# Optimization experiments

Hardware: AMD Instinct MI355X
Metric: run time of the kernel (lower is better)

The kernel has to match this reference:

```python
import jax, jax.numpy as jnp
import numpy as np

H = 128          # hidden_size
D = 128          # input_size
N_LEAVES = 262144  # 2**18 leaves -> complete binary tree, 18 reduction levels


def setup_inputs() -> dict:
    key = jax.random.key(0)
    k1, k2, k3, k4, k5 = jax.random.split(key, 5)
    s = 0.05
    return {
        "leaf_features": jax.random.normal(k1, (N_LEAVES, D), jnp.float32),
        "W_x": jax.random.normal(k2, (D, 5 * H), jnp.float32) * s,  # torch Linear weight (transposed)
        "b_x": jax.random.normal(k3, (5 * H,), jnp.float32) * s,
        "U_L": jax.random.normal(k4, (H, 5 * H), jnp.float32) * s,  # no bias, per module
        "U_R": jax.random.normal(k5, (H, 5 * H), jnp.float32) * s,
    }


def _cell(gates, left_c=None, right_c=None):
    # gates: [n, 5H] -> chunk(5, dim=1) order: i, f_L, f_R, o, u
    i, f_L, f_R, o, u = jnp.split(gates, 5, axis=1)
    c = jax.nn.sigmoid(i) * jnp.tanh(u)
    if left_c is not None:
        c = c + jax.nn.sigmoid(f_L) * left_c
    if right_c is not None:
        c = c + jax.nn.sigmoid(f_R) * right_c
    h = jax.nn.sigmoid(o) * jnp.tanh(c)
    return h, c


def reference(leaf_features, W_x, b_x, U_L, U_R):
    # Leaves: cell(feat, None, None, None, None) -> only W_x gates, all nodes batched.
    h, c = _cell(leaf_features @ W_x + b_x)  # [N_LEAVES, H]
    # Internal nodes, processed level-by-level (depth batching of the recursion).
    # Internal x = zeros -> W_x contributes only its bias b_x.
    while h.shape[0] > 1:
        gates = b_x + h[0::2] @ U_L + h[1::2] @ U_R  # [n/2, 5H]
        h, c = _cell(gates, c[0::2], c[1::2])
    return h  # root hidden state, shape (1, H)
```

## Files before the change

kernel.cpp:

```cpp
#include <hip/hip_runtime.h>
#include <hip/hip_bf16.h>
#include <stdint.h>


#define H5 640
#define HH 128
#define NLEAF 262144

typedef __attribute__((ext_vector_type(4))) float f32x4;
typedef __attribute__((ext_vector_type(8))) short bf16x8;
typedef __attribute__((ext_vector_type(4))) unsigned int u32x4;

static __device__ __forceinline__ unsigned short f2bf(float f) {
  union { float f; unsigned int i; } v; v.f = f;
  unsigned int r = v.i + 0x7FFF + ((v.i >> 16) & 1);
  return (unsigned short)(r >> 16);
}

static __device__ __forceinline__ float sigf(float x) {
  return 1.0f / (1.0f + __expf(-x));
}
static __device__ __forceinline__ float tanh_fast(float x) {
  float t = __expf(2.0f * x);
  return (t - 1.0f) / (t + 1.0f);
}

__global__ void pack_weights(const float* __restrict__ srcA,
                             const float* __restrict__ srcB,
                             int split, int KT, unsigned short* __restrict__ dst) {
  int t = blockIdx.x * blockDim.x + threadIdx.x;
  int total = 40 * KT * 64;
  if (t >= total) return;
  int lane = t & 63;
  int kf = (t >> 6) % KT;
  int nf = (t >> 6) / KT;
  int col = nf * 16 + (lane & 15);
  int k0 = kf * 32 + (lane >> 4) * 8;
  unsigned int w[4];
#pragma unroll
  for (int p = 0; p < 4; ++p) {
    int ka = k0 + 2 * p, kb = k0 + 2 * p + 1;
    float fa = (ka < split) ? srcA[(size_t)ka * H5 + col] : srcB[(size_t)(ka - split) * H5 + col];
    float fb = (kb < split) ? srcA[(size_t)kb * H5 + col] : srcB[(size_t)(kb - split) * H5 + col];
    w[p] = (unsigned int)f2bf(fa) | ((unsigned int)f2bf(fb) << 16);
  }
  u32x4* out = (u32x4*)(dst + (size_t)t * 8);
  u32x4 v; unsigned int* vp = (unsigned int*)&v;
  vp[0] = w[0]; vp[1] = w[1]; vp[2] = w[2]; vp[3] = w[3];
  *out = v;
}

__global__ void cast_leaf(const float* __restrict__ src,
                          unsigned short* __restrict__ dst, long n8) {
  long t = (long)blockIdx.x * blockDim.x + threadIdx.x;
  if (t >= n8) return;
  const float4* s = (const float4*)src + t * 2;
  float4 x = s[0], y = s[1];
  u32x4 v; unsigned int* vp = (unsigned int*)&v;
  vp[0] = (unsigned int)f2bf(x.x) | ((unsigned int)f2bf(x.y) << 16);
  vp[1] = (unsigned int)f2bf(x.z) | ((unsigned int)f2bf(x.w) << 16);
  vp[2] = (unsigned int)f2bf(y.x) | ((unsigned int)f2bf(y.y) << 16);
  vp[3] = (unsigned int)f2bf(y.z) | ((unsigned int)f2bf(y.w) << 16);
  *((u32x4*)(dst + t * 8)) = v;
}

template <int KT, bool LEAF>
__global__ __launch_bounds__(256, 2) void level_fused(
    const unsigned short* __restrict__ A,
    const unsigned short* __restrict__ Bpk,
    const float* __restrict__ bx,
    const float* __restrict__ c_child,
    unsigned short* __restrict__ h_out,
    float* __restrict__ c_out,
    float* __restrict__ h_f32_out,
    int n) {
  constexpr int K = KT * 32;
  const int lane = threadIdx.x & 63;
  const int wid = threadIdx.x >> 6;
  const int wm = wid & 1, wn = wid >> 1;
  const int row0 = blockIdx.x * 64 + wm * 32;
  const int j0 = blockIdx.y * 64 + wn * 32;

  f32x4 acc[2][2][5];
#pragma unroll
  for (int m = 0; m < 2; ++m)
#pragma unroll
    for (int nn = 0; nn < 2; ++nn)
#pragma unroll
      for (int g = 0; g < 5; ++g) acc[m][nn][g] = (f32x4)0.0f;

  const int arow = row0 + (lane & 15);
  const int kchunk = (lane >> 4) * 8;

  for (int kt = 0; kt < KT; ++kt) {
    const int k0 = kt * 32;
    bf16x8 a[2];
#pragma unroll
    for (int m = 0; m < 2; ++m)
      a[m] = *(const bf16x8*)(A + (size_t)(arow + m * 16) * K + k0 + kchunk);
#pragma unroll
    for (int g = 0; g < 5; ++g) {
#pragma unroll
      for (int nn = 0; nn < 2; ++nn) {
        const int nf = g * 8 + (j0 >> 4) + nn;
        bf16x8 b = *(const bf16x8*)(Bpk + ((size_t)(nf * KT + kt) * 64 + lane) * 8);
        acc[0][nn][g] = __builtin_amdgcn_mfma_f32_16x16x32_bf16(a[0], b, acc[0][nn][g], 0, 0, 0);
        acc[1][nn][g] = __builtin_amdgcn_mfma_f32_16x16x32_bf16(a[1], b, acc[1][nn][g], 0, 0, 0);
      }
    }
  }

  const int jc = j0 + (lane & 15);
  float bxv[5][2];
#pragma unroll
  for (int g = 0; g < 5; ++g)
#pragma unroll
    for (int nn = 0; nn < 2; ++nn) bxv[g][nn] = bx[g * 128 + jc + nn * 16];

#pragma unroll
  for (int m = 0; m < 2; ++m) {
    const int rb = row0 + m * 16 + (lane >> 4) * 4;
#pragma unroll
    for (int reg = 0; reg < 4; ++reg) {
      const int i = rb + reg;
      if (i >= n) continue;
#pragma unroll
      for (int nn = 0; nn < 2; ++nn) {
        const int j = jc + nn * 16;
        float gi = acc[m][nn][0][reg] + bxv[0][nn];
        float go = acc[m][nn][3][reg] + bxv[3][nn];
        float gu = acc[m][nn][4][reg] + bxv[4][nn];
        float c = sigf(gi) * tanh_fast(gu);
        if (!LEAF) {
          float gfL = acc[m][nn][1][reg] + bxv[1][nn];
          float gfR = acc[m][nn][2][reg] + bxv[2][nn];
          float cL = c_child[(size_t)(2 * i) * HH + j];
          float cR = c_child[(size_t)(2 * i + 1) * HH + j];
          c += sigf(gfL) * cL + sigf(gfR) * cR;
        }
        float h = sigf(go) * tanh_fast(c);
        h_out[(size_t)i * HH + j] = f2bf(h);
        c_out[(size_t)i * HH + j] = c;
        if (h_f32_out) h_f32_out[(size_t)i * HH + j] = h;
      }
    }
  }
}

extern "C" void kernel_launch(void* const* d_in, const int* in_sizes, int n_in,
                              void* d_out, int out_size, void* d_ws, size_t ws_size,
                              hipStream_t stream) {
  const float* leaf = (const float*)d_in[0];
  const float* Wx = (const float*)d_in[1];
  const float* bx = (const float*)d_in[2];
  const float* UL = (const float*)d_in[3];
  const float* UR = (const float*)d_in[4];
  float* out = (float*)d_out;

  char* ws = (char*)d_ws;
  size_t off = 0;
  auto alloc = [&](size_t bytes) -> void* {
    void* p = ws + off;
    off += (bytes + 1023) & ~(size_t)1023;
    return p;
  };
  unsigned short* Wx_pk = (unsigned short*)alloc((size_t)40 * 4 * 64 * 8 * 2);
  unsigned short* U_pk = (unsigned short*)alloc((size_t)40 * 8 * 64 * 8 * 2);
  unsigned short* leaf_bf = (unsigned short*)alloc((size_t)NLEAF * HH * 2);
  unsigned short* hA = (unsigned short*)alloc((size_t)NLEAF * HH * 2);
  unsigned short* hB = (unsigned short*)alloc((size_t)(NLEAF / 2) * HH * 2);
  float* cA = (float*)alloc((size_t)NLEAF * HH * 4);
  float* cB = (float*)alloc((size_t)(NLEAF / 2) * HH * 4);

  pack_weights<<<(40 * 4 * 64 + 255) / 256, 256, 0, stream>>>(Wx, Wx, 128, 4, Wx_pk);
  pack_weights<<<(40 * 8 * 64 + 255) / 256, 256, 0, stream>>>(UL, UR, 128, 8, U_pk);
  long n8 = (long)NLEAF * HH / 8;
  cast_leaf<<<(unsigned)(n8 / 256), 256, 0, stream>>>(leaf, leaf_bf, n8);

  level_fused<4, true><<<dim3(NLEAF / 64, 2), 256, 0, stream>>>(
      leaf_bf, Wx_pk, bx, nullptr, hA, cA, nullptr, NLEAF);

  unsigned short* hs[2] = {hA, hB};
  float* cs[2] = {cA, cB};
  int cur = 0;
  int n = NLEAF / 2;
  for (int lvl = 1; lvl <= 18; ++lvl) {
    unsigned short* hin = hs[cur];
    float* cin = cs[cur];
    unsigned short* hout = hs[cur ^ 1];
    float* cout = cs[cur ^ 1];
    float* f32out = (lvl == 18) ? out : nullptr;
    int gx = (n + 63) / 64;
    level_fused<8, false><<<dim3(gx, 2), 256, 0, stream>>>(
        hin, U_pk, bx, cin, hout, cout, f32out, n);
    cur ^= 1;
    n >>= 1;
  }
  (void)in_sizes; (void)n_in; (void)out_size; (void)ws_size;
}
```

Before: 863.0 us.

## Fuse leaf cast into GEMM, stage weights in LDS, persistent grid

Removes the separate leaf fp32-to-bf16 cast kernel and its bf16 buffer by converting leaf features in registers inside the leaf GEMM. Each block now owns one 16-column slice across all five gates, stages that slice of the packed weights in shared memory once, and loops persistently over 256-row tiles with a capped grid. This is meant to cut HBM traffic for the leaf pass and repeated global weight loads. In exchange, each block rereads A rows for its column slice (8x across blockIdx.y), and smaller levels get fewer blocks.

```diff
diff --git a/kernel.cpp b/kernel.cpp
--- a/kernel.cpp
+++ b/kernel.cpp
@@ -11,10 +11,10 @@
 typedef __attribute__((ext_vector_type(8))) short bf16x8;
 typedef __attribute__((ext_vector_type(4))) unsigned int u32x4;
 
-static __device__ __forceinline__ unsigned short f2bf(float f) {
+static __device__ __forceinline__ unsigned int f2bf(float f) {
   union { float f; unsigned int i; } v; v.f = f;
   unsigned int r = v.i + 0x7FFF + ((v.i >> 16) & 1);
-  return (unsigned short)(r >> 16);
+  return r >> 16;
 }
 
 static __device__ __forceinline__ float sigf(float x) {
@@ -42,106 +42,108 @@
     int ka = k0 + 2 * p, kb = k0 + 2 * p + 1;
     float fa = (ka < split) ? srcA[(size_t)ka * H5 + col] : srcB[(size_t)(ka - split) * H5 + col];
     float fb = (kb < split) ? srcA[(size_t)kb * H5 + col] : srcB[(size_t)(kb - split) * H5 + col];
-    w[p] = (unsigned int)f2bf(fa) | ((unsigned int)f2bf(fb) << 16);
-  }
-  u32x4* out = (u32x4*)(dst + (size_t)t * 8);
+    w[p] = f2bf(fa) | (f2bf(fb) << 16);
+  }
   u32x4 v; unsigned int* vp = (unsigned int*)&v;
   vp[0] = w[0]; vp[1] = w[1]; vp[2] = w[2]; vp[3] = w[3];
-  *out = v;
-}
-
-__global__ void cast_leaf(const float* __restrict__ src,
-                          unsigned short* __restrict__ dst, long n8) {
-  long t = (long)blockIdx.x * blockDim.x + threadIdx.x;
-  if (t >= n8) return;
-  const float4* s = (const float4*)src + t * 2;
-  float4 x = s[0], y = s[1];
-  u32x4 v; unsigned int* vp = (unsigned int*)&v;
-  vp[0] = (unsigned int)f2bf(x.x) | ((unsigned int)f2bf(x.y) << 16);
-  vp[1] = (unsigned int)f2bf(x.z) | ((unsigned int)f2bf(x.w) << 16);
-  vp[2] = (unsigned int)f2bf(y.x) | ((unsigned int)f2bf(y.y) << 16);
-  vp[3] = (unsigned int)f2bf(y.z) | ((unsigned int)f2bf(y.w) << 16);
-  *((u32x4*)(dst + t * 8)) = v;
+  *((u32x4*)(dst + (size_t)t * 8)) = v;
 }
 
 template <int KT, bool LEAF>
-__global__ __launch_bounds__(256, 2) void level_fused(
-    const unsigned short* __restrict__ A,
+__global__ __launch_bounds__(512, 4) void level_fused(
+    const void* __restrict__ Araw,
     const unsigned short* __restrict__ Bpk,
     const float* __restrict__ bx,
     const float* __restrict__ c_child,
     unsigned short* __restrict__ h_out,
     float* __restrict__ c_out,
     float* __restrict__ h_f32_out,
-    int n) {
+    int n, int NT) {
   constexpr int K = KT * 32;
+  __shared__ unsigned short smemB[5 * KT * 512];
   const int lane = threadIdx.x & 63;
   const int wid = threadIdx.x >> 6;
-  const int wm = wid & 1, wn = wid >> 1;
-  const int row0 = blockIdx.x * 64 + wm * 32;
-  const int j0 = blockIdx.y * 64 + wn * 32;
-
-  f32x4 acc[2][2][5];
-#pragma unroll
-  for (int m = 0; m < 2; ++m)
-#pragma unroll
-    for (int nn = 0; nn < 2; ++nn)
-#pragma unroll
-      for (int g = 0; g < 5; ++g) acc[m][nn][g] = (f32x4)0.0f;
-
-  const int arow = row0 + (lane & 15);
-  const int kchunk = (lane >> 4) * 8;
-
-  for (int kt = 0; kt < KT; ++kt) {
-    const int k0 = kt * 32;
-    bf16x8 a[2];
+  const int by = blockIdx.y;
+
+  {
+    const int F = 5 * KT;
+    for (int e = wid; e < F; e += 8) {
+      int g = e / KT, kt = e % KT;
+      const u32x4* src =
+          (const u32x4*)(Bpk + ((size_t)((g * 8 + by) * KT + kt) * 512) + lane * 8);
+      *((u32x4*)(smemB + e * 512 + lane * 8)) = *src;
+    }
+  }
+  __syncthreads();
+
+  const int jc = by * 16 + (lane & 15);
+  float bxv[5];
+#pragma unroll
+  for (int g = 0; g < 5; ++g) bxv[g] = bx[g * 128 + jc];
+
+  const unsigned short* Abf = (const unsigned short*)Araw;
+  const float* Af = (const float*)Araw;
+  const int kch = (lane >> 4) * 8;
+
+  for (int t = blockIdx.x; t < NT; t += gridDim.x) {
+    const int r0 = t * 256 + wid * 32 + (lane & 15);
+    f32x4 acc[2][5];
 #pragma unroll
     for (int m = 0; m < 2; ++m)
-      a[m] = *(const bf16x8*)(A + (size_t)(arow + m * 16) * K + k0 + kchunk);
-#pragma unroll
-    for (int g = 0; g < 5; ++g) {
-#pragma unroll
-      for (int nn = 0; nn < 2; ++nn) {
-        const int nf = g * 8 + (j0 >> 4) + nn;
-        bf16x8 b = *(const bf16x8*)(Bpk + ((size_t)(nf * KT + kt) * 64 + lane) * 8);
-        acc[0][nn][g] = __builtin_amdgcn_mfma_f32_16x16x32_bf16(a[0], b, acc[0][nn][g], 0, 0, 0);
-        acc[1][nn][g] = __builtin_amdgcn_mfma_f32_16x16x32_bf16(a[1], b, acc[1][nn][g], 0, 0, 0);
+#pragma unroll
+      for (int g = 0; g < 5; ++g) acc[m][g] = (f32x4)0.0f;
+
+#pragma unroll 2
+    for (int kt = 0; kt < KT; ++kt) {
+      bf16x8 a[2];
+      if (LEAF) {
+#pragma unroll
+        for (int m = 0; m < 2; ++m) {
+          const float* p = Af + (size_t)(r0 + m * 16) * K + kt * 32 + kch;
+          float4 x = *(const float4*)p;
+          float4 y = *(const float4*)(p + 4);
+          union { bf16x8 v; unsigned int u[4]; } w;
+          w.u[0] = f2bf(x.x) | (f2bf(x.y) << 16);
+          w.u[1] = f2bf(x.z) | (f2bf(x.w) << 16);
+          w.u[2] = f2bf(y.x) | (f2bf(y.y) << 16);
+          w.u[3] = f2bf(y.z) | (f2bf(y.w) << 16);
+          a[m] = w.v;
+        }
+      } else {
+#pragma unroll
+        for (int m = 0; m < 2; ++m)
+          a[m] = *(const bf16x8*)(Abf + (size_t)(r0 + m * 16) * K + kt * 32 + kch);
+      }
+#pragma unroll
+      for (int g = 0; g < 5; ++g) {
+        bf16x8 b = *(const bf16x8*)(smemB + (g * KT + kt) * 512 + lane * 8);
+        acc[0][g] = __builtin_amdgcn_mfma_f32_16x16x32_bf16(a[0], b, acc[0][g], 0, 0, 0);
+        acc[1][g] = __builtin_amdgcn_mfma_f32_16x16x32_bf16(a[1], b, acc[1][g], 0, 0, 0);
       }
     }
-  }
-
-  const int jc = j0 + (lane & 15);
-  float bxv[5][2];
-#pragma unroll
-  for (int g = 0; g < 5; ++g)
-#pragma unroll
-    for (int nn = 0; nn < 2; ++nn) bxv[g][nn] = bx[g * 128 + jc + nn * 16];
-
-#pragma unroll
-  for (int m = 0; m < 2; ++m) {
-    const int rb = row0 + m * 16 + (lane >> 4) * 4;
-#pragma unroll
-    for (int reg = 0; reg < 4; ++reg) {
-      const int i = rb + reg;
-      if (i >= n) continue;
-#pragma unroll
-      for (int nn = 0; nn < 2; ++nn) {
-        const int j = jc + nn * 16;
-        float gi = acc[m][nn][0][reg] + bxv[0][nn];
-        float go = acc[m][nn][3][reg] + bxv[3][nn];
-        float gu = acc[m][nn][4][reg] + bxv[4][nn];
+
+#pragma unroll
+    for (int m = 0; m < 2; ++m) {
+      const int ib = t * 256 + wid * 32 + m * 16 + (lane >> 4) * 4;
+#pragma unroll
+      for (int reg = 0; reg < 4; ++reg) {
+        const int i = ib + reg;
+        if (i >= n) continue;
+        float gi = acc[m][0][reg] + bxv[0];
+        float go = acc[m][3][reg] + bxv[3];
+        float gu = acc[m][4][reg] + bxv[4];
         float c = sigf(gi) * tanh_fast(gu);
         if (!LEAF) {
-          float gfL = acc[m][nn][1][reg] + bxv[1][nn];
-          float gfR = acc[m][nn][2][reg] + bxv[2][nn];
-          float cL = c_child[(size_t)(2 * i) * HH + j];
-          float cR = c_child[(size_t)(2 * i + 1) * HH + j];
+          float gfL = acc[m][1][reg] + bxv[1];
+          float gfR = acc[m][2][reg] + bxv[2];
+          float cL = c_child[(size_t)(2 * i) * HH + jc];
+          float cR = c_child[(size_t)(2 * i + 1) * HH + jc];
           c += sigf(gfL) * cL + sigf(gfR) * cR;
         }
         float h = sigf(go) * tanh_fast(c);
-        h_out[(size_t)i * HH + j] = f2bf(h);
-        c_out[(size_t)i * HH + j] = c;
-        if (h_f32_out) h_f32_out[(size_t)i * HH + j] = h;
+        h_out[(size_t)i * HH + jc] = (unsigned short)f2bf(h);
+        c_out[(size_t)i * HH + jc] = c;
+        if (h_f32_out) h_f32_out[(size_t)i * HH + jc] = h;
       }
     }
   }
@@ -166,7 +168,6 @@
   };
   unsigned short* Wx_pk = (unsigned short*)alloc((size_t)40 * 4 * 64 * 8 * 2);
   unsigned short* U_pk = (unsigned short*)alloc((size_t)40 * 8 * 64 * 8 * 2);
-  unsigned short* leaf_bf = (unsigned short*)alloc((size_t)NLEAF * HH * 2);
   unsigned short* hA = (unsigned short*)alloc((size_t)NLEAF * HH * 2);
   unsigned short* hB = (unsigned short*)alloc((size_t)(NLEAF / 2) * HH * 2);
   float* cA = (float*)alloc((size_t)NLEAF * HH * 4);
@@ -174,11 +175,13 @@
 
   pack_weights<<<(40 * 4 * 64 + 255) / 256, 256, 0, stream>>>(Wx, Wx, 128, 4, Wx_pk);
   pack_weights<<<(40 * 8 * 64 + 255) / 256, 256, 0, stream>>>(UL, UR, 128, 8, U_pk);
-  long n8 = (long)NLEAF * HH / 8;
-  cast_leaf<<<(unsigned)(n8 / 256), 256, 0, stream>>>(leaf, leaf_bf, n8);
-
-  level_fused<4, true><<<dim3(NLEAF / 64, 2), 256, 0, stream>>>(
-      leaf_bf, Wx_pk, bx, nullptr, hA, cA, nullptr, NLEAF);
+
+  {
+    int NT = NLEAF / 256;
+    int gx = 128;
+    level_fused<4, true><<<dim3(gx, 8), 512, 0, stream>>>(
+        leaf, Wx_pk, bx, nullptr, hA, cA, nullptr, NLEAF, NT);
+  }
 
   unsigned short* hs[2] = {hA, hB};
   float* cs[2] = {cA, cB};
@@ -190,9 +193,10 @@
     unsigned short* hout = hs[cur ^ 1];
     float* cout = cs[cur ^ 1];
     float* f32out = (lvl == 18) ? out : nullptr;
-    int gx = (n + 63) / 64;
-    level_fused<8, false><<<dim3(gx, 2), 256, 0, stream>>>(
-        hin, U_pk, bx, cin, hout, cout, f32out, n);
+    int NT = (n + 255) / 256;
+    int gx = NT < 96 ? NT : 96;
+    level_fused<8, false><<<dim3(gx, 8), 512, 0, stream>>>(
+        hin, U_pk, bx, cin, hout, cout, f32out, n, NT);
     cur ^= 1;
     n >>= 1;
   }
```

After: 761.4 us. -11.8%, faster.
